# Optimization experiments

Hardware: AMD Instinct MI355X
Metric: run time of the kernel (lower is better)

The kernel has to match this reference:

```python
import jax, jax.numpy as jnp
import numpy as np

SIZE = 100
NUM_PARAMS = 5
DEPTH = 10            # complete binary tree: 2**DEPTH - 1 = 1023 nodes, 512 leaves
NUM_TREES = 1024
NUM_NODES = 2 ** DEPTH - 1


def setup_inputs() -> dict:
    key = jax.random.key(0)
    ks = jax.random.split(key, 7)
    times = jax.random.uniform(ks[0], (NUM_TREES, NUM_NODES), dtype=jnp.float32) + 0.1
    # Linear(1, size): weight column vector + bias
    Qw = jax.random.normal(ks[1], (SIZE,), dtype=jnp.float32) * 0.5
    Qb = jax.random.normal(ks[2], (SIZE,), dtype=jnp.float32) * 0.1
    # Linear(size, size): scaled so deep relu chain stays stable
    Ww = jax.random.normal(ks[3], (SIZE, SIZE), dtype=jnp.float32) * (0.5 / np.sqrt(SIZE))
    Wb = jax.random.normal(ks[4], (SIZE,), dtype=jnp.float32) * 0.1
    # Linear(size, num_params)
    Pw = jax.random.normal(ks[5], (NUM_PARAMS, SIZE), dtype=jnp.float32) * (1.0 / np.sqrt(SIZE))
    Pb = jax.random.normal(ks[6], (NUM_PARAMS,), dtype=jnp.float32) * 0.1
    return {"times": times, "Qw": Qw, "Qb": Qb, "Ww": Ww, "Wb": Wb, "Pw": Pw, "Pb": Pb}


def reference(times, Qw, Qb, Ww, Wb, Pw, Pb):
    """Batched, level-synchronous version of gRNN.traverse over complete binary trees.

    times: [B, 2**D - 1] node times in heap order (node i -> children 2i+1, 2i+2).
    Leaf:     h = relu(Q(t))
    Internal: h = relu(W(h_left + h_right) + Q(t))
    Root output projected to num_params. Same math as the recursive torch code.
    """
    B, N = times.shape
    D = int(np.log2(N + 1))
    # leaf level (deepest): Q(t) = t * Qw + Qb  (Linear(1, size))
    s = 2 ** (D - 1) - 1
    h = jax.nn.relu(times[:, s:s + 2 ** (D - 1), None] * Qw + Qb)  # [B, 2^(D-1), size]
    for d in range(D - 2, -1, -1):  # fixed small loop over tree depth
        s = 2 ** d - 1
        t = times[:, s:s + 2 ** d, None]                 # [B, 2^d, 1]
        comb = h[:, 0::2] + h[:, 1::2]                   # left + right children
        h = jax.nn.relu(jnp.einsum('bns,os->bno', comb, Ww) + Wb + t * Qw + Qb)
    root = h[:, 0]                                       # [B, size]
    return root @ Pw.T + Pb                              # [B, num_params]
```

## Files before the change

### kernel.cpp

```cpp
#include <hip/hip_runtime.h>

typedef _Float16 h8 __attribute__((ext_vector_type(8)));
typedef _Float16 h4 __attribute__((ext_vector_type(4)));
typedef float f4 __attribute__((ext_vector_type(4)));
typedef unsigned int uint32;

#define NT 7
#define KC 4
#define HSTRIDE 104

__global__ __launch_bounds__(64, 1)
void grnn_fused(const float* __restrict__ times,
                const float* __restrict__ Qw,
                const float* __restrict__ Qb,
                const float* __restrict__ Ww,
                const float* __restrict__ Wb,
                const float* __restrict__ Pw,
                const float* __restrict__ Pb,
                float* __restrict__ out)
{
  __shared__ __align__(16) _Float16 Cs[128][HSTRIDE];
  __shared__ __align__(8)  _Float16 ts[1026];
  __shared__ __align__(16) float qw_s[128];
  __shared__ __align__(16) float qb_s[128];

  const int lane = threadIdx.x;
  const int l15  = lane & 15;
  const int kg   = lane >> 4;
  const int tree = blockIdx.x;

  {
    const float* tg = times + tree * 1023;
    #pragma unroll
    for (int i = 0; i < 16; ++i) {
      const int idx = lane + 64 * i;
      if (idx < 1023) ts[1 + idx] = (_Float16)tg[idx];
    }
    if (lane == 0) ts[0] = (_Float16)0.f;
    #pragma unroll
    for (int i = 0; i < 2; ++i) {
      const int idx = lane + 64 * i;
      float qw = 0.f, qb = 0.f;
      if (idx < 100) { qw = Qw[idx]; qb = Qb[idx]; }
      qw_s[idx] = qw; qb_s[idx] = qb;
    }
  }

  h8 wf[NT][KC];
  #pragma unroll
  for (int nt = 0; nt < NT; ++nt) {
    const int r = nt * 16 + l15;
    #pragma unroll
    for (int kc = 0; kc < KC; ++kc) {
      h8 v;
      #pragma unroll
      for (int j = 0; j < 8; ++j) v[j] = (_Float16)0.f;
      if (r < 100) {
        const int kb = kc * 32 + kg * 8;
        if (kc < 3) {
          const f4 w0 = *(const f4*)&Ww[r * 100 + kb];
          const f4 w1 = *(const f4*)&Ww[r * 100 + kb + 4];
          #pragma unroll
          for (int j = 0; j < 4; ++j) {
            v[j]     = (_Float16)w0[j];
            v[j + 4] = (_Float16)w1[j];
          }
        } else if (kg == 0) {
          const f4 w0 = *(const f4*)&Ww[r * 100 + 96];
          #pragma unroll
          for (int j = 0; j < 4; ++j) v[j] = (_Float16)w0[j];
          v[4] = (_Float16)Qw[r];
          v[5] = (_Float16)(Qb[r] + Wb[r]);
        }
      }
      wf[nt][kc] = v;
    }
  }

#define DO_MT(MT) do {                                                        \
    _Pragma("unroll")                                                         \
    for (int nt_ = 0; nt_ < NT; ++nt_) {                                      \
      f4 acc_ = {0.f, 0.f, 0.f, 0.f};                                         \
      _Pragma("unroll")                                                       \
      for (int kc_ = 0; kc_ < KC; ++kc_)                                      \
        acc_ = __builtin_amdgcn_mfma_f32_16x16x32_f16(wf[nt_][kc_],           \
                                                      af[kc_], acc_, 0,0,0);  \
      if (nt_ < 6 || kg == 0) {                                               \
        h4 hv_ = {(_Float16)fmaxf(acc_[0], 0.f),                              \
                  (_Float16)fmaxf(acc_[1], 0.f),                              \
                  (_Float16)fmaxf(acc_[2], 0.f),                              \
                  (_Float16)fmaxf(acc_[3], 0.f)};                             \
        uint2 u_ = __builtin_bit_cast(uint2, hv_);                            \
        u_.x = __shfl_xor(u_.x, 1, 64);                                       \
        u_.y = __shfl_xor(u_.y, 1, 64);                                       \
        hv_ = hv_ + __builtin_bit_cast(h4, u_);                               \
        if ((l15 & 1) == 0)                                                   \
          *(h4*)&Cs[(MT) * 8 + (l15 >> 1)][nt_ * 16 + kg * 4] = hv_;          \
      }                                                                       \
    }                                                                         \
  } while (0)

#define DO_MT_ROOT() do {                                                     \
    _Pragma("unroll")                                                         \
    for (int nt_ = 0; nt_ < NT; ++nt_) {                                      \
      f4 acc_ = {0.f, 0.f, 0.f, 0.f};                                         \
      _Pragma("unroll")                                                       \
      for (int kc_ = 0; kc_ < KC; ++kc_)                                      \
        acc_ = __builtin_amdgcn_mfma_f32_16x16x32_f16(wf[nt_][kc_],           \
                                                      af[kc_], acc_, 0,0,0);  \
      if ((nt_ < 6 || kg == 0) && l15 == 0) {                                 \
        h4 hv_ = {(_Float16)fmaxf(acc_[0], 0.f),                              \
                  (_Float16)fmaxf(acc_[1], 0.f),                              \
                  (_Float16)fmaxf(acc_[2], 0.f),                              \
                  (_Float16)fmaxf(acc_[3], 0.f)};                             \
        *(h4*)&Cs[0][nt_ * 16 + kg * 4] = hv_;                                \
      }                                                                       \
    }                                                                         \
  } while (0)

#define LOAD_AFR(MT, S) do {                                                  \
    const int row_ = (MT) * 16 + l15;                                         \
    _Pragma("unroll")                                                         \
    for (int kc_ = 0; kc_ < 3; ++kc_)                                         \
      af[kc_] = *(const h8*)&Cs[row_][kc_ * 32 + kg * 8];                     \
    if (kg == 0) {                                                            \
      h4 lo_ = *(const h4*)&Cs[row_][96];                                     \
      h4 hi_ = {ts[1 + (S) + (MT) * 16 + l15], (_Float16)1.f,                 \
                (_Float16)0.f, (_Float16)0.f};                                \
      af[3] = __builtin_shufflevector(lo_, hi_, 0, 1, 2, 3, 4, 5, 6, 7);      \
    } else {                                                                  \
      _Pragma("unroll")                                                       \
      for (int j_ = 0; j_ < 8; ++j_) af[3][j_] = (_Float16)0.f;               \
    }                                                                         \
  } while (0)

  #pragma unroll 1
  for (int i = 0; i < 16; ++i) {
    const int m = i * 16 + l15;
    const uint32 tp = *(const uint32*)&ts[512 + 2 * m];
    const float t0 = (float)*(const _Float16*)&tp;
    const float t1 = (float)*((const _Float16*)&tp + 1);
    h8 af[KC];
    #pragma unroll
    for (int kc = 0; kc < KC; ++kc) {
      const int kb = kc * 32 + kg * 8;
      const f4 qwa = *(const f4*)&qw_s[kb];
      const f4 qwb = *(const f4*)&qw_s[kb + 4];
      const f4 qba = *(const f4*)&qb_s[kb];
      const f4 qbb = *(const f4*)&qb_s[kb + 4];
      #pragma unroll
      for (int j = 0; j < 4; ++j) {
        float h0 = fmaxf(t0 * qwa[j] + qba[j], 0.f);
        float h1 = fmaxf(t1 * qwa[j] + qba[j], 0.f);
        af[kc][j] = (_Float16)(h0 + h1);
        float g0 = fmaxf(t0 * qwb[j] + qbb[j], 0.f);
        float g1 = fmaxf(t1 * qwb[j] + qbb[j], 0.f);
        af[kc][j + 4] = (_Float16)(g0 + g1);
      }
    }
    if (kg == 0) {
      af[3][4] = ts[1 + 255 + m];
      af[3][5] = (_Float16)1.f;
      af[3][6] = (_Float16)0.f;
      af[3][7] = (_Float16)0.f;
    }
    DO_MT(i);
  }

  #pragma unroll 1
  for (int d = 7; d >= 1; --d) {
    const int s  = (1 << d) - 1;
    const int nm = (d >= 4) ? (1 << (d - 4)) : 1;
    #pragma unroll 1
    for (int i = 0; i < nm; ++i) {
      h8 af[KC];
      LOAD_AFR(i, s);
      DO_MT(i);
    }
  }

  {
    h8 af[KC];
    LOAD_AFR(0, 0);
    DO_MT_ROOT();
  }

  #pragma unroll 1
  for (int p = 0; p < 5; ++p) {
    float v = (float)Cs[0][lane] * Pw[p * 100 + lane];
    if (lane < 36) v += (float)Cs[0][64 + lane] * Pw[p * 100 + 64 + lane];
    v += __shfl_xor(v, 32, 64);
    v += __shfl_xor(v, 16, 64);
    v += __shfl_xor(v, 8, 64);
    v += __shfl_xor(v, 4, 64);
    v += __shfl_xor(v, 2, 64);
    v += __shfl_xor(v, 1, 64);
    if (lane == 0) out[tree * 5 + p] = v + Pb[p];
  }
#undef DO_MT
#undef DO_MT_ROOT
#undef LOAD_AFR
}

extern "C" void kernel_launch(void* const* d_in, const int* in_sizes, int n_in,
                              void* d_out, int out_size, void* d_ws, size_t ws_size,
                              hipStream_t stream) {
  (void)n_in; (void)out_size; (void)d_ws; (void)ws_size;
  const float* times = (const float*)d_in[0];
  const float* Qw = (const float*)d_in[1];
  const float* Qb = (const float*)d_in[2];
  const float* Ww = (const float*)d_in[3];
  const float* Wb = (const float*)d_in[4];
  const float* Pw = (const float*)d_in[5];
  const float* Pb = (const float*)d_in[6];
  float* outp = (float*)d_out;
  const int B = in_sizes[0] / 1023;
  grnn_fused<<<dim3(B), dim3(64), 0, stream>>>(times, Qw, Qb, Ww, Wb, Pw, Pb, outp);
}
```

Baseline: 112.5 us.

## Prefetch next tile's A-fragments, use packed fp16 leaf math and branchless stores

Flattens the level/tile loops into a single software-pipelined schedule that loads the next tile's A fragments from LDS while the current tile's MFMAs run. Leaf-level math moves to packed fp16 vectors held in registers instead of fp32 reads from LDS. The shuffle reduction is replaced with DPP quad-permute moves, and predicated stores are replaced with unconditional stores redirected to a trash buffer. This cuts LDS latency stalls and branch overhead, but leaf activations now carry fp16 rounding and register pressure rises. Pipelining across levels relies on the single wavefront's program order to keep LDS reads and writes correctly ordered.

```diff
diff --git a/kernel.cpp b/kernel.cpp
--- a/kernel.cpp
+++ b/kernel.cpp
@@ -2,8 +2,8 @@
 
 typedef _Float16 h8 __attribute__((ext_vector_type(8)));
 typedef _Float16 h4 __attribute__((ext_vector_type(4)));
+typedef _Float16 h2 __attribute__((ext_vector_type(2)));
 typedef float f4 __attribute__((ext_vector_type(4)));
-typedef unsigned int uint32;
 
 #define NT 7
 #define KC 4
@@ -20,9 +20,9 @@
                 float* __restrict__ out)
 {
   __shared__ __align__(16) _Float16 Cs[128][HSTRIDE];
-  __shared__ __align__(8)  _Float16 ts[1026];
-  __shared__ __align__(16) float qw_s[128];
-  __shared__ __align__(16) float qb_s[128];
+  __shared__ __align__(16) _Float16 trash[512];
+  __shared__ __align__(4)  _Float16 ts_fold[512];
+  __shared__ __align__(4)  h2 tsp[256];
 
   const int lane = threadIdx.x;
   const int l15  = lane & 15;
@@ -32,17 +32,10 @@
   {
     const float* tg = times + tree * 1023;
     #pragma unroll
-    for (int i = 0; i < 16; ++i) {
-      const int idx = lane + 64 * i;
-      if (idx < 1023) ts[1 + idx] = (_Float16)tg[idx];
-    }
-    if (lane == 0) ts[0] = (_Float16)0.f;
-    #pragma unroll
-    for (int i = 0; i < 2; ++i) {
-      const int idx = lane + 64 * i;
-      float qw = 0.f, qb = 0.f;
-      if (idx < 100) { qw = Qw[idx]; qb = Qb[idx]; }
-      qw_s[idx] = qw; qb_s[idx] = qb;
+    for (int q = 0; q < 4; ++q) {
+      const int pr = lane + 64 * q;
+      *(h2*)&ts_fold[2 * pr] = (h2){(_Float16)tg[2 * pr], (_Float16)tg[2 * pr + 1]};
+      tsp[pr] = (h2){(_Float16)tg[511 + 2 * pr], (_Float16)tg[512 + 2 * pr]};
     }
   }
 
@@ -77,113 +70,123 @@
     }
   }
 
-#define DO_MT(MT) do {                                                        \
+  h8 qwp[KC], qbp[KC];
+  #pragma unroll
+  for (int kc = 0; kc < KC; ++kc) {
+    const int kb = kc * 32 + kg * 8;
+    #pragma unroll
+    for (int j = 0; j < 8; ++j) {
+      const int ix = kb + j;
+      qwp[kc][j] = (ix < 100) ? (_Float16)Qw[ix] : (_Float16)0.f;
+      qbp[kc][j] = (ix < 100) ? (_Float16)Qb[ix] : (_Float16)0.f;
+    }
+  }
+
+#define DO_MT(AFR, MT) do {                                                   \
+    const int rw_ = (MT) * 8 + (l15 >> 1);                                    \
+    _Float16* pv_ = (l15 & 1) ? &trash[lane * 4] : &Cs[rw_][kg * 4];          \
+    _Float16* p6_ = kg ? &trash[lane * 4] : pv_;                              \
     _Pragma("unroll")                                                         \
     for (int nt_ = 0; nt_ < NT; ++nt_) {                                      \
       f4 acc_ = {0.f, 0.f, 0.f, 0.f};                                         \
       _Pragma("unroll")                                                       \
       for (int kc_ = 0; kc_ < KC; ++kc_)                                      \
         acc_ = __builtin_amdgcn_mfma_f32_16x16x32_f16(wf[nt_][kc_],           \
-                                                      af[kc_], acc_, 0,0,0);  \
-      if (nt_ < 6 || kg == 0) {                                               \
-        h4 hv_ = {(_Float16)fmaxf(acc_[0], 0.f),                              \
-                  (_Float16)fmaxf(acc_[1], 0.f),                              \
-                  (_Float16)fmaxf(acc_[2], 0.f),                              \
-                  (_Float16)fmaxf(acc_[3], 0.f)};                             \
-        uint2 u_ = __builtin_bit_cast(uint2, hv_);                            \
-        u_.x = __shfl_xor(u_.x, 1, 64);                                       \
-        u_.y = __shfl_xor(u_.y, 1, 64);                                       \
-        hv_ = hv_ + __builtin_bit_cast(h4, u_);                               \
-        if ((l15 & 1) == 0)                                                   \
-          *(h4*)&Cs[(MT) * 8 + (l15 >> 1)][nt_ * 16 + kg * 4] = hv_;          \
-      }                                                                       \
+                                                      AFR[kc_], acc_, 0,0,0); \
+      h2 c0_ = {(_Float16)acc_[0], (_Float16)acc_[1]};                        \
+      h2 c1_ = {(_Float16)acc_[2], (_Float16)acc_[3]};                        \
+      const h2 z2_ = {(_Float16)0.f, (_Float16)0.f};                          \
+      c0_ = __builtin_elementwise_max(c0_, z2_);                              \
+      c1_ = __builtin_elementwise_max(c1_, z2_);                              \
+      int d0_ = __builtin_amdgcn_mov_dpp(__builtin_bit_cast(int, c0_),        \
+                                         0xB1, 0xF, 0xF, true);               \
+      int d1_ = __builtin_amdgcn_mov_dpp(__builtin_bit_cast(int, c1_),        \
+                                         0xB1, 0xF, 0xF, true);               \
+      c0_ = c0_ + __builtin_bit_cast(h2, d0_);                                \
+      c1_ = c1_ + __builtin_bit_cast(h2, d1_);                                \
+      h4 hv_ = {c0_[0], c0_[1], c1_[0], c1_[1]};                              \
+      *(h4*)((nt_ == 6 ? p6_ : pv_) + nt_ * 16) = hv_;                        \
     }                                                                         \
   } while (0)
 
-#define DO_MT_ROOT() do {                                                     \
+#define DO_MT_ROOT(AFR) do {                                                  \
+    _Float16* pv_ = (l15 == 0) ? &Cs[0][kg * 4] : &trash[lane * 4];           \
+    _Float16* p6_ = kg ? &trash[lane * 4] : pv_;                              \
     _Pragma("unroll")                                                         \
     for (int nt_ = 0; nt_ < NT; ++nt_) {                                      \
       f4 acc_ = {0.f, 0.f, 0.f, 0.f};                                         \
       _Pragma("unroll")                                                       \
       for (int kc_ = 0; kc_ < KC; ++kc_)                                      \
         acc_ = __builtin_amdgcn_mfma_f32_16x16x32_f16(wf[nt_][kc_],           \
-                                                      af[kc_], acc_, 0,0,0);  \
-      if ((nt_ < 6 || kg == 0) && l15 == 0) {                                 \
-        h4 hv_ = {(_Float16)fmaxf(acc_[0], 0.f),                              \
-                  (_Float16)fmaxf(acc_[1], 0.f),                              \
-                  (_Float16)fmaxf(acc_[2], 0.f),                              \
-                  (_Float16)fmaxf(acc_[3], 0.f)};                             \
-        *(h4*)&Cs[0][nt_ * 16 + kg * 4] = hv_;                                \
-      }                                                                       \
+                                                      AFR[kc_], acc_, 0,0,0); \
+      h2 c0_ = {(_Float16)acc_[0], (_Float16)acc_[1]};                        \
+      h2 c1_ = {(_Float16)acc_[2], (_Float16)acc_[3]};                        \
+      const h2 z2_ = {(_Float16)0.f, (_Float16)0.f};                          \
+      c0_ = __builtin_elementwise_max(c0_, z2_);                              \
+      c1_ = __builtin_elementwise_max(c1_, z2_);                              \
+      h4 hv_ = {c0_[0], c0_[1], c1_[0], c1_[1]};                              \
+      *(h4*)((nt_ == 6 ? p6_ : pv_) + nt_ * 16) = hv_;                        \
     }                                                                         \
   } while (0)
 
-#define LOAD_AFR(MT, S) do {                                                  \
+#define LOAD_AFR(AFR, MT, S) do {                                             \
     const int row_ = (MT) * 16 + l15;                                         \
-    _Pragma("unroll")                                                         \
-    for (int kc_ = 0; kc_ < 3; ++kc_)                                         \
-      af[kc_] = *(const h8*)&Cs[row_][kc_ * 32 + kg * 8];                     \
-    if (kg == 0) {                                                            \
-      h4 lo_ = *(const h4*)&Cs[row_][96];                                     \
-      h4 hi_ = {ts[1 + (S) + (MT) * 16 + l15], (_Float16)1.f,                 \
-                (_Float16)0.f, (_Float16)0.f};                                \
-      af[3] = __builtin_shufflevector(lo_, hi_, 0, 1, 2, 3, 4, 5, 6, 7);      \
-    } else {                                                                  \
-      _Pragma("unroll")                                                       \
-      for (int j_ = 0; j_ < 8; ++j_) af[3][j_] = (_Float16)0.f;               \
-    }                                                                         \
+    AFR[0] = *(const h8*)&Cs[row_][kg * 8];                                   \
+    AFR[1] = *(const h8*)&Cs[row_][32 + kg * 8];                              \
+    AFR[2] = *(const h8*)&Cs[row_][64 + kg * 8];                              \
+    h4 lo_ = *(const h4*)&Cs[row_][96];                                       \
+    h4 hi_ = {ts_fold[(S) + (MT) * 16 + l15], (_Float16)1.f,                  \
+              (_Float16)0.f, (_Float16)0.f};                                  \
+    AFR[3] = __builtin_shufflevector(lo_, hi_, 0, 1, 2, 3, 4, 5, 6, 7);       \
   } while (0)
 
-  #pragma unroll 1
+  const h8 z8 = {(_Float16)0.f, (_Float16)0.f, (_Float16)0.f, (_Float16)0.f,
+                 (_Float16)0.f, (_Float16)0.f, (_Float16)0.f, (_Float16)0.f};
+  #pragma unroll 2
   for (int i = 0; i < 16; ++i) {
     const int m = i * 16 + l15;
-    const uint32 tp = *(const uint32*)&ts[512 + 2 * m];
-    const float t0 = (float)*(const _Float16*)&tp;
-    const float t1 = (float)*((const _Float16*)&tp + 1);
-    h8 af[KC];
+    const h2 tp = tsp[m];
+    const _Float16 t0 = tp[0], t1 = tp[1];
+    h8 afl[KC];
     #pragma unroll
     for (int kc = 0; kc < KC; ++kc) {
-      const int kb = kc * 32 + kg * 8;
-      const f4 qwa = *(const f4*)&qw_s[kb];
-      const f4 qwb = *(const f4*)&qw_s[kb + 4];
-      const f4 qba = *(const f4*)&qb_s[kb];
-      const f4 qbb = *(const f4*)&qb_s[kb + 4];
-      #pragma unroll
-      for (int j = 0; j < 4; ++j) {
-        float h0 = fmaxf(t0 * qwa[j] + qba[j], 0.f);
-        float h1 = fmaxf(t1 * qwa[j] + qba[j], 0.f);
-        af[kc][j] = (_Float16)(h0 + h1);
-        float g0 = fmaxf(t0 * qwb[j] + qbb[j], 0.f);
-        float g1 = fmaxf(t1 * qwb[j] + qbb[j], 0.f);
-        af[kc][j + 4] = (_Float16)(g0 + g1);
-      }
-    }
-    if (kg == 0) {
-      af[3][4] = ts[1 + 255 + m];
-      af[3][5] = (_Float16)1.f;
-      af[3][6] = (_Float16)0.f;
-      af[3][7] = (_Float16)0.f;
-    }
-    DO_MT(i);
-  }
-
+      h8 a = qwp[kc] * t0 + qbp[kc];
+      h8 b = qwp[kc] * t1 + qbp[kc];
+      a = __builtin_elementwise_max(a, z8);
+      b = __builtin_elementwise_max(b, z8);
+      afl[kc] = a + b;
+    }
+    afl[3][4] = ts_fold[255 + m];
+    afl[3][5] = (_Float16)1.f;
+    DO_MT(afl, i);
+  }
+
+  h8 af[KC], afn[KC];
+  LOAD_AFR(af, 0, 127);
   #pragma unroll 1
-  for (int d = 7; d >= 1; --d) {
-    const int s  = (1 << d) - 1;
-    const int nm = (d >= 4) ? (1 << (d - 4)) : 1;
-    #pragma unroll 1
-    for (int i = 0; i < nm; ++i) {
-      h8 af[KC];
-      LOAD_AFR(i, s);
-      DO_MT(i);
-    }
-  }
-
-  {
-    h8 af[KC];
-    LOAD_AFR(0, 0);
-    DO_MT_ROOT();
-  }
+  for (int j = 0; j < 14; ++j) {
+    const int i = j - ((j < 8) ? 0 : (j < 12) ? 8 : 12);
+    if (j < 13) {
+      const int j2 = j + 1;
+      const int d2 = (j2 < 8) ? 7 : (j2 < 12) ? 6 : 5;
+      const int i2 = j2 - ((j2 < 8) ? 0 : (j2 < 12) ? 8 : 12);
+      LOAD_AFR(afn, i2, (1 << d2) - 1);
+    }
+    DO_MT(af, i);
+    if (j == 13) LOAD_AFR(afn, 0, 15);
+    #pragma unroll
+    for (int c = 0; c < KC; ++c) af[c] = afn[c];
+  }
+
+  #pragma unroll 1
+  for (int d = 4; d >= 1; --d) {
+    DO_MT(af, 0);
+    LOAD_AFR(afn, 0, (1 << (d - 1)) - 1);
+    #pragma unroll
+    for (int c = 0; c < KC; ++c) af[c] = afn[c];
+  }
+
+  DO_MT_ROOT(af);
 
   #pragma unroll 1
   for (int p = 0; p < 5; ++p) {
```

New measurement: 94.05 us. 16.4% less time.
